# Kernel tuning notes

Measured on AMD Instinct MI355X. Metric: run time of the kernel, lower is better.

Reference implementation:

```python
import jax, jax.numpy as jnp
import numpy as np

NEG_SLOPE = 0.2


def _gatv2_layer(x, src, dst, Wl, Wr, att, b, n):
    """GATv2Conv, heads=1, concat=True, share_weights=False (PyG semantics).
    src -> source nodes (messages flow src->dst), dst -> target nodes.
    e_ij = att . leaky_relu(Wl x_j + Wr x_i); softmax over incoming edges of i;
    out_i = sum_j alpha_ij * (Wl x_j) + b.
    """
    xl = x @ Wl                     # [N, C]  (source transform)
    xr = x @ Wr                     # [N, C]  (target transform)
    e = jax.nn.leaky_relu(xl[src] + xr[dst], NEG_SLOPE)  # [E, C]
    logits = e @ att                # [E]
    # segment softmax over destination nodes (self-loops guarantee nonempty segments)
    m = jax.ops.segment_max(logits, dst, num_segments=n)
    a = jnp.exp(logits - m[dst])
    denom = jax.ops.segment_sum(a, dst, num_segments=n)
    alpha = a / denom[dst]          # [E]
    out = jax.ops.segment_sum(alpha[:, None] * xl[src], dst, num_segments=n)
    return out + b


def setup_inputs() -> dict:
    key = jax.random.key(0)
    ks = jax.random.split(key, 12)
    n, e, f, h1, h2, c = 50000, 800000, 128, 256, 128, 40

    def glorot(k, shape, fan_in):
        return (jax.random.normal(k, shape, dtype=jnp.float32) / np.float32(np.sqrt(fan_in)))

    x = jax.random.normal(ks[0], (n, f), dtype=jnp.float32)
    edge_index = jax.random.randint(ks[1], (2, e), 0, n, dtype=jnp.int32)
    return {
        "x": x,
        "edge_index": edge_index,
        "W1l": glorot(ks[2], (f, h1), f),
        "W1r": glorot(ks[3], (f, h1), f),
        "att1": glorot(ks[4], (h1,), h1),
        "b1": jnp.zeros((h1,), dtype=jnp.float32),
        "W2l": glorot(ks[5], (h1, h2), h1),
        "W2r": glorot(ks[6], (h1, h2), h1),
        "att2": glorot(ks[7], (h2,), h2),
        "b2": jnp.zeros((h2,), dtype=jnp.float32),
        "Wc": glorot(ks[8], (h2, c), h2),
        "bc": jnp.zeros((c,), dtype=jnp.float32),
    }


def reference(x, edge_index, W1l, W1r, att1, b1, W2l, W2r, att2, b2, Wc, bc):
    n = x.shape[0]
    # GATv2Conv default add_self_loops=True
    loop = jnp.arange(n, dtype=edge_index.dtype)
    src = jnp.concatenate([edge_index[0], loop])
    dst = jnp.concatenate([edge_index[1], loop])
    h = jax.nn.relu(_gatv2_layer(x, src, dst, W1l, W1r, att1, b1, n))
    h = jax.nn.relu(_gatv2_layer(h, src, dst, W2l, W2r, att2, b2, n))
    return h @ Wc + bc
```

## Files before the change

kernel.cpp:

```cpp
#include <hip/hip_runtime.h>
#include <math.h>

#define NEG_SLOPE 0.2f

typedef __attribute__((ext_vector_type(8))) short short8;
typedef __attribute__((ext_vector_type(4))) float f32x4;

__device__ __forceinline__ void split2(float f, short& hi, short& lo)
{
    unsigned u  = __float_as_uint(f);
    unsigned hu = u & 0xffff0000u;
    hi = (short)(hu >> 16);
    float r = f - __uint_as_float(hu);
    unsigned ru = __float_as_uint(r);
    unsigned rnd = ru + 0x7fffu + ((ru >> 16) & 1u);
    lo = (short)(rnd >> 16);
}

__device__ __forceinline__ unsigned short bf16rne(float f)
{
    unsigned u = __float_as_uint(f);
    unsigned rnd = u + 0x7fffu + ((u >> 16) & 1u);
    return (unsigned short)(rnd >> 16);
}

__device__ __forceinline__ float bf2f(unsigned short h)
{
    return __uint_as_float(((unsigned)h) << 16);
}

__global__ void k_degree(const int* __restrict__ ei, int E, int n, int* __restrict__ deg)
{
    int e = blockIdx.x * blockDim.x + threadIdx.x;
    int etot = E + n;
    if (e < etot) {
        int dst = (e < E) ? ei[E + e] : (e - E);
        atomicAdd(&deg[dst], 1);
    }
}

#define SCAN_BLK 1024
__global__ void k_scan1(const int* __restrict__ deg, int* __restrict__ scanned,
                        int* __restrict__ sums, int n)
{
    __shared__ int sh[SCAN_BLK];
    int base = blockIdx.x * SCAN_BLK;
    int t = threadIdx.x;
    int v = (base + t < n) ? deg[base + t] : 0;
    sh[t] = v;
    __syncthreads();
    for (int off = 1; off < SCAN_BLK; off <<= 1) {
        int x = (t >= off) ? sh[t - off] : 0;
        __syncthreads();
        sh[t] += x;
        __syncthreads();
    }
    if (base + t < n) scanned[base + t] = sh[t];
    if (t == SCAN_BLK - 1) sums[blockIdx.x] = sh[t];
}

__global__ void k_scan2(int* __restrict__ sums, int nb)
{
    if (threadIdx.x == 0 && blockIdx.x == 0) {
        int run = 0;
        for (int i = 0; i < nb; ++i) { int v = sums[i]; sums[i] = run; run += v; }
    }
}

__global__ void k_scan3(const int* __restrict__ scanned, const int* __restrict__ sums,
                        const int* __restrict__ deg, int* __restrict__ indptr,
                        int* __restrict__ cursor, int n)
{
    int i = blockIdx.x * blockDim.x + threadIdx.x;
    if (i < n) {
        int incl = scanned[i] + sums[i / SCAN_BLK];
        indptr[i + 1] = incl;
        cursor[i] = incl - deg[i];
        if (i == 0) indptr[0] = 0;
    }
}

__global__ void k_scatter(const int* __restrict__ ei, int E, int n,
                          int* __restrict__ cursor, int* __restrict__ csr_src)
{
    int e = blockIdx.x * blockDim.x + threadIdx.x;
    int etot = E + n;
    if (e < etot) {
        int src, dst;
        if (e < E) { src = ei[e]; dst = ei[E + e]; }
        else       { src = dst = e - E; }
        int pos = atomicAdd(&cursor[dst], 1);
        csr_src[pos] = src;
    }
}

__global__ void k_split_a(const float* __restrict__ X, short* __restrict__ A2,
                          long total4, int K)
{
    long t = (long)blockIdx.x * blockDim.x + threadIdx.x;
    if (t >= total4) return;
    long i = t * 4;
    int row = (int)(i / K);
    int k   = (int)(i % K);
    float4 v = *reinterpret_cast<const float4*>(X + i);
    short4 hi, lo;
    split2(v.x, hi.x, lo.x); split2(v.y, hi.y, lo.y);
    split2(v.z, hi.z, lo.z); split2(v.w, hi.w, lo.w);
    short* base = A2 + (size_t)row * 2 * K + ((k >> 5) << 6) + (k & 31);
    *reinterpret_cast<short4*>(base)      = hi;
    *reinterpret_cast<short4*>(base + 32) = lo;
}

__global__ void k_split_bt(const float* __restrict__ Wa, const float* __restrict__ Wb,
                           int Na, int Nb, int K, short* __restrict__ Bt)
{
    int idx = blockIdx.x * blockDim.x + threadIdx.x;
    int N = Na + Nb;
    if (idx >= N * K) return;
    int j = idx / K, k = idx % K;
    float v = (j < Na) ? Wa[(size_t)k * Na + j] : Wb[(size_t)k * Nb + (j - Na)];
    short hi, lo;
    split2(v, hi, lo);
    short* base = Bt + (size_t)j * 2 * K + ((k >> 5) << 6) + (k & 31);
    base[0]  = hi;
    base[32] = lo;
}

template<int BN, bool BF16OUT>
__global__ __launch_bounds__(256) void k_mfma(
    const short* __restrict__ A2, const short* __restrict__ Bt,
    const float* __restrict__ bias, void* __restrict__ Cout,
    int M, int N, int K)
{
    constexpr int NI  = BN / 32;
    constexpr int NBI = BN / 8;
    __shared__ __align__(16) char lds[(128 + BN) * 128];

    const int tid  = threadIdx.x;
    const int lane = tid & 63;
    const int wid  = tid >> 6;
    const int wr   = wid >> 1;
    const int wc   = wid & 1;
    const int bm   = blockIdx.y * 128;
    const int bn   = blockIdx.x * BN;
    const size_t rowb = (size_t)4 * K;

    f32x4 acc[4][NI] = {};
    const int lrow = lane & 15;
    const int c0   = lane >> 4;
    const char* A2b = (const char*)A2;
    const char* Btb = (const char*)Bt;

    for (int kc = 0; kc < (K >> 5); ++kc) {
        for (int i = wid; i < 16 + NBI; i += 4) {
            bool isA = i < 16;
            int  i0  = isA ? i : i - 16;
            int  row = i0 * 8 + (lane >> 3);
            int  s   = lane & 7;
            int  sd  = s ^ (row & 7);
            int  gr  = (isA ? bm : bn) + row;
            int  gmax = (isA ? M : N) - 1;
            if (gr > gmax) gr = gmax;
            const char* src = (isA ? A2b : Btb) + (size_t)gr * rowb + kc * 128 + sd * 16;
            int dstoff = (isA ? 0 : 16384) + i0 * 1024;
            __builtin_amdgcn_global_load_lds((const void*)src, (void*)&lds[dstoff], 16, 0, 0);
        }
        __syncthreads();

        short8 ah[4], al[4], bh[NI], bl[NI];
        #pragma unroll
        for (int mi = 0; mi < 4; ++mi) {
            int rl = wr * 64 + mi * 16 + lrow;
            int ch = c0 ^ (rl & 7);
            int cl = (c0 + 4) ^ (rl & 7);
            ah[mi] = *reinterpret_cast<const short8*>(&lds[rl * 128 + ch * 16]);
            al[mi] = *reinterpret_cast<const short8*>(&lds[rl * 128 + cl * 16]);
        }
        #pragma unroll
        for (int ni = 0; ni < NI; ++ni) {
            int rl = wc * (BN / 2) + ni * 16 + lrow;
            int ch = c0 ^ (rl & 7);
            int cl = (c0 + 4) ^ (rl & 7);
            bh[ni] = *reinterpret_cast<const short8*>(&lds[16384 + rl * 128 + ch * 16]);
            bl[ni] = *reinterpret_cast<const short8*>(&lds[16384 + rl * 128 + cl * 16]);
        }

        #pragma unroll
        for (int mi = 0; mi < 4; ++mi)
            #pragma unroll
            for (int ni = 0; ni < NI; ++ni) {
                acc[mi][ni] = __builtin_amdgcn_mfma_f32_16x16x32_bf16(ah[mi], bh[ni], acc[mi][ni], 0, 0, 0);
                acc[mi][ni] = __builtin_amdgcn_mfma_f32_16x16x32_bf16(ah[mi], bl[ni], acc[mi][ni], 0, 0, 0);
                acc[mi][ni] = __builtin_amdgcn_mfma_f32_16x16x32_bf16(al[mi], bh[ni], acc[mi][ni], 0, 0, 0);
            }
        __syncthreads();
    }

    #pragma unroll
    for (int mi = 0; mi < 4; ++mi)
        #pragma unroll
        for (int ni = 0; ni < NI; ++ni) {
            int row0 = bm + wr * 64 + mi * 16 + (lane >> 4) * 4;
            int col  = bn + wc * (BN / 2) + ni * 16 + (lane & 15);
            if (col >= N) continue;
            float badd = bias ? bias[col] : 0.f;
            #pragma unroll
            for (int q = 0; q < 4; ++q) {
                int row = row0 + q;
                if (row >= M) continue;
                float v = acc[mi][ni][q] + badd;
                if (BF16OUT)
                    ((unsigned short*)Cout)[(size_t)row * N + col] = bf16rne(v);
                else
                    ((float*)Cout)[(size_t)row * N + col] = v;
            }
        }
}

template<int VEC>
__global__ __launch_bounds__(256) void k_fused(
    const unsigned short* __restrict__ xlr, int ldx, int xroff,
    const int* __restrict__ csr_src, const int* __restrict__ indptr,
    const float* __restrict__ att, const float* __restrict__ bias,
    short* __restrict__ outs, int n)
{
    const int C = VEC * 64;
    const int lane = threadIdx.x & 63;
    const int node = blockIdx.x * 4 + (threadIdx.x >> 6);
    if (node >= n) return;
    const int beg = indptr[node], end = indptr[node + 1];

    float attr[VEC], xri[VEC];
    if constexpr (VEC == 4) {
        float4 a = *reinterpret_cast<const float4*>(att + lane * 4);
        attr[0] = a.x; attr[1] = a.y; attr[2] = a.z; attr[3] = a.w;
        ushort4 r = *reinterpret_cast<const ushort4*>(xlr + (size_t)node * ldx + xroff + lane * 4);
        xri[0] = bf2f(r.x); xri[1] = bf2f(r.y); xri[2] = bf2f(r.z); xri[3] = bf2f(r.w);
    } else {
        float2 a = *reinterpret_cast<const float2*>(att + lane * 2);
        attr[0] = a.x; attr[1] = a.y;
        ushort2 r = *reinterpret_cast<const ushort2*>(xlr + (size_t)node * ldx + xroff + lane * 2);
        xri[0] = bf2f(r.x); xri[1] = bf2f(r.y);
    }

    float m = -3.4e38f, s = 0.f;
    float acc[VEC] = {};

    for (int base = beg; base < end; base += 64) {
        const int len = (end - base < 64) ? (end - base) : 64;
        int csr = (base + lane < end) ? csr_src[base + lane] : 0;

        uint2 vb_n = make_uint2(0u, 0u);
        unsigned vb1_n = 0u;
        {
            int s0 = __shfl(csr, 0);
            if constexpr (VEC == 4)
                vb_n = *reinterpret_cast<const uint2*>(xlr + (size_t)s0 * ldx + lane * 4);
            else
                vb1_n = *reinterpret_cast<const unsigned*>(xlr + (size_t)s0 * ldx + lane * 2);
        }

        for (int j = 0; j < len; ++j) {
            float v[VEC];
            if constexpr (VEC == 4) {
                uint2 vb = vb_n;
                if (j + 1 < len) {
                    int s2 = __shfl(csr, j + 1);
                    vb_n = *reinterpret_cast<const uint2*>(xlr + (size_t)s2 * ldx + lane * 4);
                }
                v[0] = bf2f((unsigned short)(vb.x & 0xffffu));
                v[1] = bf2f((unsigned short)(vb.x >> 16));
                v[2] = bf2f((unsigned short)(vb.y & 0xffffu));
                v[3] = bf2f((unsigned short)(vb.y >> 16));
            } else {
                unsigned vb = vb1_n;
                if (j + 1 < len) {
                    int s2 = __shfl(csr, j + 1);
                    vb1_n = *reinterpret_cast<const unsigned*>(xlr + (size_t)s2 * ldx + lane * 2);
                }
                v[0] = bf2f((unsigned short)(vb & 0xffffu));
                v[1] = bf2f((unsigned short)(vb >> 16));
            }

            float p = 0.f;
            #pragma unroll
            for (int i = 0; i < VEC; ++i) {
                float t = v[i] + xri[i];
                t = t > 0.f ? t : NEG_SLOPE * t;
                p += attr[i] * t;
            }
            #pragma unroll
            for (int off = 1; off < 64; off <<= 1) p += __shfl_xor(p, off);

            float newm = fmaxf(m, p);
            float sc = __expf(m - newm);
            float w  = __expf(p - newm);
            m = newm;
            s = s * sc + w;
            #pragma unroll
            for (int i = 0; i < VEC; ++i) acc[i] = acc[i] * sc + w * v[i];
        }
    }

    float inv = 1.f / s;
    int cbase = lane * VEC;
    short hi[VEC], lo[VEC];
    #pragma unroll
    for (int i = 0; i < VEC; ++i) {
        float o = fmaxf(acc[i] * inv + bias[cbase + i], 0.f);
        split2(o, hi[i], lo[i]);
    }
    short* obase = outs + (size_t)node * 2 * C + ((cbase >> 5) << 6) + (cbase & 31);
    if constexpr (VEC == 4) {
        *reinterpret_cast<short4*>(obase)      = make_short4(hi[0], hi[1], hi[2], hi[3]);
        *reinterpret_cast<short4*>(obase + 32) = make_short4(lo[0], lo[1], lo[2], lo[3]);
    } else {
        *reinterpret_cast<short2*>(obase)      = make_short2(hi[0], hi[1]);
        *reinterpret_cast<short2*>(obase + 32) = make_short2(lo[0], lo[1]);
    }
}

extern "C" void kernel_launch(void* const* d_in, const int* in_sizes, int n_in,
                              void* d_out, int out_size, void* d_ws, size_t ws_size,
                              hipStream_t stream)
{
    const float* x    = (const float*)d_in[0];
    const int*   ei   = (const int*)d_in[1];
    const float* W1l  = (const float*)d_in[2];
    const float* W1r  = (const float*)d_in[3];
    const float* att1 = (const float*)d_in[4];
    const float* b1   = (const float*)d_in[5];
    const float* W2l  = (const float*)d_in[6];
    const float* W2r  = (const float*)d_in[7];
    const float* att2 = (const float*)d_in[8];
    const float* b2   = (const float*)d_in[9];
    const float* Wc   = (const float*)d_in[10];
    const float* bc   = (const float*)d_in[11];

    const int h1 = in_sizes[4];
    const int h2 = in_sizes[8];
    const int c  = in_sizes[11];
    const int f  = in_sizes[2] / h1;
    const int n  = in_sizes[0] / f;
    const int E  = in_sizes[1] / 2;
    const int Etot = E + n;

    char* p = (char*)d_ws;
    auto alloc = [&](size_t bytes) -> char* {
        char* r = p; p += (bytes + 255) & ~(size_t)255; return r;
    };
    unsigned short* xlr1 = (unsigned short*)alloc((size_t)n * 2 * h1 * 2);
    short* hsplit1 = (short*)alloc((size_t)n * 2 * h1 * 2);
    short* a2x     = (short*)alloc((size_t)n * 2 * f * 2);
    short* bt1     = (short*)alloc((size_t)(2 * h1) * (2 * f) * 2);
    short* bt2     = (short*)alloc((size_t)(2 * h2) * (2 * h1) * 2);
    short* btc     = (short*)alloc((size_t)c * (2 * h2) * 2);
    int*   csr_src = (int*)alloc((size_t)Etot * 4);
    int*   indptr  = (int*)alloc((size_t)(n + 1) * 4);
    int*   cursor  = (int*)alloc((size_t)n * 4);
    int*   deg     = (int*)alloc((size_t)n * 4);
    int*   scanned = (int*)alloc((size_t)n * 4);
    int*   sums    = (int*)alloc(4096);

    unsigned short* xlr2 = xlr1;
    short* hsplit2 = a2x;

    const int tb = 256;

    long total4 = (long)n * f / 4;
    k_split_a<<<(int)((total4 + tb - 1) / tb), tb, 0, stream>>>(x, a2x, total4, f);
    k_split_bt<<<(2 * h1 * f + tb - 1) / tb, tb, 0, stream>>>(W1l, W1r, h1, h1, f, bt1);
    k_split_bt<<<(2 * h2 * h1 + tb - 1) / tb, tb, 0, stream>>>(W2l, W2r, h2, h2, h1, bt2);
    k_split_bt<<<(c * h2 + tb - 1) / tb, tb, 0, stream>>>(Wc, nullptr, c, 0, h2, btc);

    hipMemsetAsync(deg, 0, (size_t)n * 4, stream);
    k_degree<<<(Etot + tb - 1) / tb, tb, 0, stream>>>(ei, E, n, deg);
    int nb = (n + SCAN_BLK - 1) / SCAN_BLK;
    k_scan1<<<nb, SCAN_BLK, 0, stream>>>(deg, scanned, sums, n);
    k_scan2<<<1, 64, 0, stream>>>(sums, nb);
    k_scan3<<<(n + tb - 1) / tb, tb, 0, stream>>>(scanned, sums, deg, indptr, cursor, n);
    k_scatter<<<(Etot + tb - 1) / tb, tb, 0, stream>>>(ei, E, n, cursor, csr_src);

    const int gy = (n + 127) / 128;

    k_mfma<128, true><<<dim3((2 * h1 + 127) / 128, gy), 256, 0, stream>>>(
        a2x, bt1, nullptr, xlr1, n, 2 * h1, f);
    k_fused<4><<<(n + 3) / 4, 256, 0, stream>>>(
        xlr1, 2 * h1, h1, csr_src, indptr, att1, b1, hsplit1, n);

    k_mfma<128, true><<<dim3((2 * h2 + 127) / 128, gy), 256, 0, stream>>>(
        hsplit1, bt2, nullptr, xlr2, n, 2 * h2, h1);
    k_fused<2><<<(n + 3) / 4, 256, 0, stream>>>(
        xlr2, 2 * h2, h2, csr_src, indptr, att2, b2, hsplit2, n);

    k_mfma<64, false><<<dim3((c + 63) / 64, gy), 256, 0, stream>>>(
        hsplit2, btc, bc, d_out, n, c, h2);
}
```

Measured before the change: 480.4 us.

## Pack multiple destination nodes per wavefront in fused GATv2 aggregation

```diff
diff --git a/kernel.cpp b/kernel.cpp
--- a/kernel.cpp
+++ b/kernel.cpp
@@ -24,10 +24,8 @@
     return (unsigned short)(rnd >> 16);
 }
 
-__device__ __forceinline__ float bf2f(unsigned short h)
-{
-    return __uint_as_float(((unsigned)h) << 16);
-}
+__device__ __forceinline__ float bf2f_lo(unsigned u) { return __uint_as_float(u << 16); }
+__device__ __forceinline__ float bf2f_hi(unsigned u) { return __uint_as_float(u & 0xffff0000u); }
 
 __global__ void k_degree(const int* __restrict__ ei, int E, int n, int* __restrict__ deg)
 {
@@ -217,106 +215,103 @@
         }
 }
 
-template<int VEC>
+template<int NSUB>
 __global__ __launch_bounds__(256) void k_fused(
     const unsigned short* __restrict__ xlr, int ldx, int xroff,
     const int* __restrict__ csr_src, const int* __restrict__ indptr,
     const float* __restrict__ att, const float* __restrict__ bias,
     short* __restrict__ outs, int n)
 {
-    const int C = VEC * 64;
+    constexpr int LSUB = 64 / NSUB;
+    constexpr int C = 8 * LSUB;
     const int lane = threadIdx.x & 63;
-    const int node = blockIdx.x * 4 + (threadIdx.x >> 6);
-    if (node >= n) return;
-    const int beg = indptr[node], end = indptr[node + 1];
-
-    float attr[VEC], xri[VEC];
-    if constexpr (VEC == 4) {
-        float4 a = *reinterpret_cast<const float4*>(att + lane * 4);
-        attr[0] = a.x; attr[1] = a.y; attr[2] = a.z; attr[3] = a.w;
-        ushort4 r = *reinterpret_cast<const ushort4*>(xlr + (size_t)node * ldx + xroff + lane * 4);
-        xri[0] = bf2f(r.x); xri[1] = bf2f(r.y); xri[2] = bf2f(r.z); xri[3] = bf2f(r.w);
-    } else {
-        float2 a = *reinterpret_cast<const float2*>(att + lane * 2);
-        attr[0] = a.x; attr[1] = a.y;
-        ushort2 r = *reinterpret_cast<const ushort2*>(xlr + (size_t)node * ldx + xroff + lane * 2);
-        xri[0] = bf2f(r.x); xri[1] = bf2f(r.y);
+    const int wid  = threadIdx.x >> 6;
+    const int sub  = lane / LSUB;
+    const int sl   = lane % LSUB;
+    const int node = blockIdx.x * (4 * NSUB) + wid * NSUB + sub;
+    const bool valid = node < n;
+    const int nodec = valid ? node : 0;
+    const int beg = indptr[nodec];
+    const int end = valid ? indptr[nodec + 1] : beg;
+
+    float attr[8], xri[8];
+    {
+        float4 a0 = *reinterpret_cast<const float4*>(att + sl * 8);
+        float4 a1 = *reinterpret_cast<const float4*>(att + sl * 8 + 4);
+        attr[0]=a0.x; attr[1]=a0.y; attr[2]=a0.z; attr[3]=a0.w;
+        attr[4]=a1.x; attr[5]=a1.y; attr[6]=a1.z; attr[7]=a1.w;
+        uint4 r = *reinterpret_cast<const uint4*>(xlr + (size_t)nodec * ldx + xroff + sl * 8);
+        xri[0]=bf2f_lo(r.x); xri[1]=bf2f_hi(r.x);
+        xri[2]=bf2f_lo(r.y); xri[3]=bf2f_hi(r.y);
+        xri[4]=bf2f_lo(r.z); xri[5]=bf2f_hi(r.z);
+        xri[6]=bf2f_lo(r.w); xri[7]=bf2f_hi(r.w);
     }
 
     float m = -3.4e38f, s = 0.f;
-    float acc[VEC] = {};
-
-    for (int base = beg; base < end; base += 64) {
-        const int len = (end - base < 64) ? (end - base) : 64;
-        int csr = (base + lane < end) ? csr_src[base + lane] : 0;
-
-        uint2 vb_n = make_uint2(0u, 0u);
-        unsigned vb1_n = 0u;
-        {
-            int s0 = __shfl(csr, 0);
-            if constexpr (VEC == 4)
-                vb_n = *reinterpret_cast<const uint2*>(xlr + (size_t)s0 * ldx + lane * 4);
-            else
-                vb1_n = *reinterpret_cast<const unsigned*>(xlr + (size_t)s0 * ldx + lane * 2);
-        }
-
-        for (int j = 0; j < len; ++j) {
-            float v[VEC];
-            if constexpr (VEC == 4) {
-                uint2 vb = vb_n;
-                if (j + 1 < len) {
-                    int s2 = __shfl(csr, j + 1);
-                    vb_n = *reinterpret_cast<const uint2*>(xlr + (size_t)s2 * ldx + lane * 4);
+    float acc[8] = {};
+
+    int deg = end - beg;
+    int mdeg = deg;
+    if constexpr (NSUB == 4) mdeg = max(mdeg, __shfl_xor(mdeg, 16));
+    mdeg = max(mdeg, __shfl_xor(mdeg, 32));
+    const int nch = (mdeg + LSUB - 1) / LSUB;
+
+    for (int it = 0; it < nch; ++it) {
+        const int base = beg + it * LSUB;
+        int len = end - base;
+        len = len < 0 ? 0 : (len > LSUB ? LSUB : len);
+        const int csr = (sl < len) ? csr_src[base + sl] : 0;
+        int wlen = len;
+        if constexpr (NSUB == 4) wlen = max(wlen, __shfl_xor(wlen, 16));
+        wlen = max(wlen, __shfl_xor(wlen, 32));
+
+        for (int j = 0; j < wlen; ++j) {
+            const bool active = j < len;
+            const int src = __shfl(csr, sub * LSUB + j);
+            float v[8];
+            float p = 0.f;
+            if (active) {
+                uint4 vb = *reinterpret_cast<const uint4*>(xlr + (size_t)src * ldx + sl * 8);
+                v[0]=bf2f_lo(vb.x); v[1]=bf2f_hi(vb.x);
+                v[2]=bf2f_lo(vb.y); v[3]=bf2f_hi(vb.y);
+                v[4]=bf2f_lo(vb.z); v[5]=bf2f_hi(vb.z);
+                v[6]=bf2f_lo(vb.w); v[7]=bf2f_hi(vb.w);
+                #pragma unroll
+                for (int i = 0; i < 8; ++i) {
+                    float t = v[i] + xri[i];
+                    t = fmaxf(t, NEG_SLOPE * t);
+                    p += attr[i] * t;
                 }
-                v[0] = bf2f((unsigned short)(vb.x & 0xffffu));
-                v[1] = bf2f((unsigned short)(vb.x >> 16));
-                v[2] = bf2f((unsigned short)(vb.y & 0xffffu));
-                v[3] = bf2f((unsigned short)(vb.y >> 16));
-            } else {
-                unsigned vb = vb1_n;
-                if (j + 1 < len) {
-                    int s2 = __shfl(csr, j + 1);
-                    vb1_n = *reinterpret_cast<const unsigned*>(xlr + (size_t)s2 * ldx + lane * 2);
-                }
-                v[0] = bf2f((unsigned short)(vb & 0xffffu));
-                v[1] = bf2f((unsigned short)(vb >> 16));
-            }
-
-            float p = 0.f;
-            #pragma unroll
-            for (int i = 0; i < VEC; ++i) {
-                float t = v[i] + xri[i];
-                t = t > 0.f ? t : NEG_SLOPE * t;
-                p += attr[i] * t;
             }
             #pragma unroll
-            for (int off = 1; off < 64; off <<= 1) p += __shfl_xor(p, off);
-
-            float newm = fmaxf(m, p);
-            float sc = __expf(m - newm);
-            float w  = __expf(p - newm);
-            m = newm;
-            s = s * sc + w;
-            #pragma unroll
-            for (int i = 0; i < VEC; ++i) acc[i] = acc[i] * sc + w * v[i];
-        }
-    }
-
-    float inv = 1.f / s;
-    int cbase = lane * VEC;
-    short hi[VEC], lo[VEC];
-    #pragma unroll
-    for (int i = 0; i < VEC; ++i) {
-        float o = fmaxf(acc[i] * inv + bias[cbase + i], 0.f);
-        split2(o, hi[i], lo[i]);
-    }
-    short* obase = outs + (size_t)node * 2 * C + ((cbase >> 5) << 6) + (cbase & 31);
-    if constexpr (VEC == 4) {
-        *reinterpret_cast<short4*>(obase)      = make_short4(hi[0], hi[1], hi[2], hi[3]);
-        *reinterpret_cast<short4*>(obase + 32) = make_short4(lo[0], lo[1], lo[2], lo[3]);
-    } else {
-        *reinterpret_cast<short2*>(obase)      = make_short2(hi[0], hi[1]);
-        *reinterpret_cast<short2*>(obase + 32) = make_short2(lo[0], lo[1]);
+            for (int off = 1; off < LSUB; off <<= 1) p += __shfl_xor(p, off);
+
+            if (active) {
+                float newm = fmaxf(m, p);
+                float sc = __expf(m - newm);
+                float w  = __expf(p - newm);
+                m = newm;
+                s = s * sc + w;
+                #pragma unroll
+                for (int i = 0; i < 8; ++i) acc[i] = acc[i] * sc + w * v[i];
+            }
+        }
+    }
+
+    if (valid) {
+        float inv = 1.f / s;
+        int cbase = sl * 8;
+        short hi[8], lo[8];
+        #pragma unroll
+        for (int i = 0; i < 8; ++i) {
+            float o = fmaxf(acc[i] * inv + bias[cbase + i], 0.f);
+            split2(o, hi[i], lo[i]);
+        }
+        short* obase = outs + (size_t)node * 2 * C + ((cbase >> 5) << 6) + (cbase & 31);
+        *reinterpret_cast<short4*>(obase)          = make_short4(hi[0], hi[1], hi[2], hi[3]);
+        *reinterpret_cast<short4*>(obase + 4)      = make_short4(hi[4], hi[5], hi[6], hi[7]);
+        *reinterpret_cast<short4*>(obase + 32)     = make_short4(lo[0], lo[1], lo[2], lo[3]);
+        *reinterpret_cast<short4*>(obase + 36)     = make_short4(lo[4], lo[5], lo[6], lo[7]);
     }
 }
 
@@ -385,12 +380,12 @@
 
     k_mfma<128, true><<<dim3((2 * h1 + 127) / 128, gy), 256, 0, stream>>>(
         a2x, bt1, nullptr, xlr1, n, 2 * h1, f);
-    k_fused<4><<<(n + 3) / 4, 256, 0, stream>>>(
+    k_fused<2><<<(n + 7) / 8, 256, 0, stream>>>(
         xlr1, 2 * h1, h1, csr_src, indptr, att1, b1, hsplit1, n);
 
     k_mfma<128, true><<<dim3((2 * h2 + 127) / 128, gy), 256, 0, stream>>>(
         hsplit1, bt2, nullptr, xlr2, n, 2 * h2, h1);
-    k_fused<2><<<(n + 3) / 4, 256, 0, stream>>>(
+    k_fused<4><<<(n + 15) / 16, 256, 0, stream>>>(
         xlr2, 2 * h2, h2, csr_src, indptr, att2, b2, hsplit2, n);
 
     k_mfma<64, false><<<dim3((c + 63) / 64, gy), 256, 0, stream>>>(
```

Result: faster. 447.9 us (-6.8%).
